# Performance work log

Measured on AMD Instinct MI355X. Metric: run time of the kernel, lower is better.

The kernel has to match this reference:

```python
import jax, jax.numpy as jnp
import numpy as np

B, SE, T, S, D, V = 64, 128, 64, 1024, 1024, 32000


def setup_inputs() -> dict:
    key = jax.random.key(0)
    ks = jax.random.split(key, 24)
    w = lambda k, shp: jax.random.normal(k, shp, jnp.float32) * 0.02
    return {
        "encoder_yts": jax.random.normal(ks[0], (B, SE, S), jnp.float32),
        "encoder_h": jax.random.normal(ks[1], (B, S), jnp.float32),
        "tgt": jax.random.randint(ks[2], (B, T), 0, V),
        "emb": w(ks[3], (V, D)),
        "asi_w": w(ks[4], (S, S)), "asi_b": jnp.zeros((S,), jnp.float32),
        "ayi_w": w(ks[5], (S, S)), "ayi_b": jnp.zeros((S,), jnp.float32),
        "aw_w": w(ks[6], (S, 1)), "aw_b": jnp.zeros((1,), jnp.float32),
        "wf_w": w(ks[7], (S, S)), "wf_b": jnp.zeros((S,), jnp.float32),
        "uf_w": w(ks[8], (D, S)), "uf_b": jnp.zeros((S,), jnp.float32),
        "wi_w": w(ks[9], (S, S)), "wi_b": jnp.zeros((S,), jnp.float32),
        "ui_w": w(ks[10], (D, S)), "ui_b": jnp.zeros((S,), jnp.float32),
        "wo_w": w(ks[11], (S, S)), "wo_b": jnp.zeros((S,), jnp.float32),
        "uo_w": w(ks[12], (D, S)), "uo_b": jnp.zeros((S,), jnp.float32),
        "wc_w": w(ks[13], (S, S)), "wc_b": jnp.zeros((S,), jnp.float32),
        "uc_w": w(ks[14], (D, S)), "uc_b": jnp.zeros((S,), jnp.float32),
        "xh_w": w(ks[15], (S, D)), "xh_b": jnp.zeros((D,), jnp.float32),
        "cls_w": w(ks[16], (D, V)), "cls_b": jnp.zeros((V,), jnp.float32),
    }


def reference(encoder_yts, encoder_h, tgt, emb,
              asi_w, asi_b, ayi_w, ayi_b, aw_w, aw_b,
              wf_w, wf_b, uf_w, uf_b, wi_w, wi_b, ui_w, ui_b,
              wo_w, wo_b, uo_w, uo_b, wc_w, wc_b, uc_w, uc_b,
              xh_w, xh_b, cls_w, cls_b):
    # Teacher-forced decode: xt at step i is the embedding of tgt[:, i].
    # Precompute attention key projection of encoder outputs: [B, SE, S]
    yts_proj = encoder_yts @ ayi_w + ayi_b
    xs = jnp.transpose(emb[tgt], (1, 0, 2))  # [T, B, D]

    def step(st, xt):
        # Additive attention (no tanh, matches source): e_ij = w^T(W si + U y)
        q = st @ asi_w + asi_b                       # [B, S]
        e = ((q[:, None, :] + yts_proj) @ aw_w)[..., 0] + aw_b[0]  # [B, SE]
        attn = jax.nn.softmax(e, axis=-1)            # [B, SE]
        ctx = jnp.einsum('be,bed->bd', attn, encoder_yts)  # [B, S] cell input
        # LSTM cell: note ct_1 is the fresh attention context each step
        ft = jax.nn.sigmoid(st @ wf_w + wf_b + xt @ uf_w + uf_b)
        it = jax.nn.sigmoid(st @ wi_w + wi_b + xt @ ui_w + ui_b)
        ot = jax.nn.sigmoid(st @ wo_w + wo_b + xt @ uo_w + uo_b)
        cbar = jnp.tanh(st @ wc_w + wc_b + xt @ uc_w + uc_b)
        ct = ft * ctx + it * cbar
        ht = ot * jnp.tanh(ct)                       # [B, S] -> next st
        logits = (ht @ xh_w + xh_b) @ cls_w + cls_b  # [B, V]
        pt = jax.nn.softmax(logits, axis=-1)
        return ht, (pt, attn)

    _, (pts, attns) = jax.lax.scan(step, encoder_h, xs)
    # [T,B,V] -> [B,T,V]; [T,B,SE] -> [B,T,SE]
    return jnp.transpose(pts, (1, 0, 2)), jnp.transpose(attns, (1, 0, 2))
```

## Files before the change

### kernel.cpp

```cpp
#include <hip/hip_runtime.h>
#include <cstdint>
#include <cstddef>

#define B_  64
#define SE_ 128
#define T_  64
#define S_  1024
#define D_  1024
#define V_  32000

typedef __attribute__((ext_vector_type(8))) short bhalf8;
typedef __attribute__((ext_vector_type(4))) float floatx4;

__device__ __forceinline__ float sigmoidf_(float x){ return 1.0f/(1.0f+__expf(-x)); }

__device__ __forceinline__ ushort f2bf(float f){
  uint32_t u = __float_as_uint(f);
  uint32_t r = (u + 0x7fffu + ((u >> 16) & 1u)) >> 16;
  return (ushort)r;
}
__device__ __forceinline__ float bf2f(ushort h){ return __uint_as_float(((uint32_t)h) << 16); }

__device__ __forceinline__ void glds16(const ushort* g, ushort* l){
  __builtin_amdgcn_global_load_lds((const __attribute__((address_space(1))) void*)g,
                                   (__attribute__((address_space(3))) void*)l, 16, 0, 0);
}

__device__ __forceinline__ float waveRedSum(float v){
  #pragma unroll
  for (int off = 32; off; off >>= 1) v += __shfl_down(v, off, 64);
  return v;
}


__global__ void k_attnvec(const float* __restrict__ ayi_w, const float* __restrict__ aw_w,
                          float* __restrict__ v){
  int wave = (blockIdx.x * blockDim.x + threadIdx.x) >> 6;
  int lane = threadIdx.x & 63;
  if (wave >= S_) return;
  const float* row = ayi_w + (size_t)wave * S_;
  float acc = 0.f;
  #pragma unroll 4
  for (int s = lane; s < S_; s += 64) acc += row[s] * aw_w[s];
  acc = waveRedSum(acc);
  if (lane == 0) v[wave] = acc;
}

__global__ void k_scores(const float* __restrict__ yts, const float* __restrict__ v,
                         float* __restrict__ scores){
  int wave = (blockIdx.x * blockDim.x + threadIdx.x) >> 6;
  int lane = threadIdx.x & 63;
  const float* row = yts + (size_t)wave * S_;
  float acc = 0.f;
  #pragma unroll 4
  for (int s = lane; s < S_; s += 64) acc += row[s] * v[s];
  acc = waveRedSum(acc);
  if (lane == 0) scores[wave] = acc;
}

__global__ void k_attn(const float* __restrict__ scores, float* __restrict__ attnw,
                       float* __restrict__ outAttn){
  int b = blockIdx.x;
  int e = threadIdx.x;
  __shared__ float sm[128];
  float x = scores[b*SE_ + e];
  sm[e] = x; __syncthreads();
  #pragma unroll
  for (int off = 64; off; off >>= 1){
    if (e < off) sm[e] = fmaxf(sm[e], sm[e+off]);
    __syncthreads();
  }
  float m = sm[0]; __syncthreads();
  float p = __expf(x - m);
  sm[e] = p; __syncthreads();
  #pragma unroll
  for (int off = 64; off; off >>= 1){
    if (e < off) sm[e] += sm[e+off];
    __syncthreads();
  }
  float a = p / sm[0];
  attnw[b*SE_ + e] = a;
  float* dst = outAttn + (size_t)b * T_ * SE_ + e;
  #pragma unroll 4
  for (int t = 0; t < T_; ++t) dst[t*SE_] = a;
}

__global__ void k_ctx(const float* __restrict__ yts, const float* __restrict__ attnw,
                      float* __restrict__ ctx){
  int idx = blockIdx.x * blockDim.x + threadIdx.x;
  int b = idx >> 10, s = idx & (S_-1);
  const float* base = yts + (size_t)b * SE_ * S_ + s;
  const float* a = attnw + b * SE_;
  float acc = 0.f;
  #pragma unroll 8
  for (int e = 0; e < SE_; ++e) acc += a[e] * base[(size_t)e * S_];
  ctx[idx] = acc;
}


__global__ void k_transcvt(const float* __restrict__ src, ushort* __restrict__ dst,
                           int K, int N){
  __shared__ float t[32][33];
  int n0 = blockIdx.x * 32, k0 = blockIdx.y * 32;
  for (int r = threadIdx.y; r < 32; r += 8)
    t[r][threadIdx.x] = src[(size_t)(k0 + r) * N + n0 + threadIdx.x];
  __syncthreads();
  for (int r = threadIdx.y; r < 32; r += 8)
    dst[(size_t)(n0 + r) * K + k0 + threadIdx.x] = f2bf(t[threadIdx.x][r]);
}

__global__ void k_cvt(const float* __restrict__ src, ushort* __restrict__ dst, int n4){
  int i = blockIdx.x * blockDim.x + threadIdx.x;
  if (i >= n4) return;
  float4 v = ((const float4*)src)[i];
  ushort4 o; o.x = f2bf(v.x); o.y = f2bf(v.y); o.z = f2bf(v.z); o.w = f2bf(v.w);
  ((ushort4*)dst)[i] = o;
}

__global__ void k_gathercvt(const float* __restrict__ emb, const int* __restrict__ tgt,
                            ushort* __restrict__ Xb){
  int r = blockIdx.x;
  int token = tgt[((r & 63) << 6) + (r >> 6)];
  const float4* src = (const float4*)(emb + (size_t)token * D_);
  ushort* dst = Xb + (size_t)r * D_;
  int i = threadIdx.x;
  float4 v = src[i];
  ushort4 o; o.x = f2bf(v.x); o.y = f2bf(v.y); o.z = f2bf(v.z); o.w = f2bf(v.w);
  ((ushort4*)dst)[i] = o;
}

__global__ void k_packbias(const float* __restrict__ wb0, const float* __restrict__ wb1,
                           const float* __restrict__ wb2, const float* __restrict__ wb3,
                           const float* __restrict__ ub0, const float* __restrict__ ub1,
                           const float* __restrict__ ub2, const float* __restrict__ ub3,
                           float* __restrict__ dst){
  int col = blockIdx.x * blockDim.x + threadIdx.x;
  int g = col >> 10, s = col & 1023;
  const float* wb = (g==0) ? wb0 : (g==1) ? wb1 : (g==2) ? wb2 : wb3;
  const float* ub = (g==0) ? ub0 : (g==1) ? ub1 : (g==2) ? ub2 : ub3;
  dst[col] = wb[s] + ub[s];
}

template<int OUT_MODE>
__global__ __launch_bounds__(256) void k_mfma_gemm(
    const ushort* __restrict__ A, const ushort* __restrict__ BT,
    const float* __restrict__ bias, void* __restrict__ C, int M, int N)
{
  __shared__ ushort As[128*32];
  __shared__ ushort Bs[128*32];
  const int tid = threadIdx.x;
  const int lane = tid & 63, w = tid >> 6;
  const int m0 = blockIdx.y * 128, n0 = blockIdx.x * 128;
  const int wr = (w >> 1) * 64, wc = (w & 1) * 64;

  const int cr = (lane >> 2);
  const int ck = (lane & 3) * 8;
  const ushort* gA0 = A  + (size_t)(m0 + (2*w)*16   + cr) * 1024 + ck;
  const ushort* gA1 = A  + (size_t)(m0 + (2*w+1)*16 + cr) * 1024 + ck;
  const ushort* gB0 = BT + (size_t)(n0 + (2*w)*16   + cr) * 1024 + ck;
  const ushort* gB1 = BT + (size_t)(n0 + (2*w+1)*16 + cr) * 1024 + ck;
  ushort* lA0 = As + (2*w)*512;   ushort* lA1 = As + (2*w+1)*512;
  ushort* lB0 = Bs + (2*w)*512;   ushort* lB1 = Bs + (2*w+1)*512;

  floatx4 acc[4][4] = {};

  for (int kt = 0; kt < 1024; kt += 32) {
    glds16(gA0 + kt, lA0); glds16(gA1 + kt, lA1);
    glds16(gB0 + kt, lB0); glds16(gB1 + kt, lB1);
    __syncthreads();
    bhalf8 a[4], b[4];
    #pragma unroll
    for (int f = 0; f < 4; ++f) {
      a[f] = *(const bhalf8*)&As[(wr + f*16 + (lane & 15)) * 32 + (lane >> 4) * 8];
      b[f] = *(const bhalf8*)&Bs[(wc + f*16 + (lane & 15)) * 32 + (lane >> 4) * 8];
    }
    #pragma unroll
    for (int i = 0; i < 4; ++i)
      #pragma unroll
      for (int j = 0; j < 4; ++j)
        acc[i][j] = __builtin_amdgcn_mfma_f32_16x16x32_bf16(a[i], b[j], acc[i][j], 0, 0, 0);
    __syncthreads();
  }

  const int crow = (lane >> 4) * 4, ccol = lane & 15;
  #pragma unroll
  for (int i = 0; i < 4; ++i) {
    #pragma unroll
    for (int j = 0; j < 4; ++j) {
      int row = m0 + wr + i*16 + crow;
      int col = n0 + wc + j*16 + ccol;
      float bv = bias ? bias[col] : 0.f;
      #pragma unroll
      for (int r = 0; r < 4; ++r) {
        float v = acc[i][j][r] + bv;
        if (OUT_MODE == 0) {
          ((float*)C)[(size_t)(row + r) * N + col] = v;
        } else if (OUT_MODE == 1) {
          int rr = row + r;
          ((float*)C)[(size_t)(((rr & 63) << 6) + (rr >> 6)) * N + col] = v;
        } else {
          ((ushort*)C)[(size_t)(row + r) * N + col] = f2bf(v);
        }
      }
    }
  }
}

__global__ __launch_bounds__(256) void k_step(
    const ushort* __restrict__ Hin,
    const ushort* __restrict__ WT,
    const ushort* __restrict__ preb,
    const float*  __restrict__ ctx,
    ushort* __restrict__ Hout)
{
  __shared__ ushort As[64*32];
  __shared__ ushort Bs[4][64*32];
  __shared__ float gbuf[4][64][66];
  const int tid = threadIdx.x, lane = tid & 63, w = tid >> 6;
  const int j = blockIdx.x;

  const int cr = (lane >> 2);
  const int ck = (lane & 3) * 8;
  const ushort* gA = Hin + (size_t)(w*16 + cr) * 1024 + ck;
  ushort* lA = As + w*512;
  const ushort* gB = WT + (size_t)(w*1024 + j*64 + cr) * 1024 + ck;
  ushort* lB = Bs[w];

  floatx4 acc[4][4] = {};

  for (int kt = 0; kt < 1024; kt += 32) {
    glds16(gA + kt, lA);
    #pragma unroll
    for (int c = 0; c < 4; ++c)
      glds16(gB + (size_t)(c*16)*1024 + kt, lB + c*512);
    __syncthreads();
    bhalf8 a[4], b[4];
    #pragma unroll
    for (int f = 0; f < 4; ++f) {
      a[f] = *(const bhalf8*)&As[(f*16 + (lane & 15)) * 32 + (lane >> 4) * 8];
      b[f] = *(const bhalf8*)&Bs[w][(f*16 + (lane & 15)) * 32 + (lane >> 4) * 8];
    }
    #pragma unroll
    for (int i = 0; i < 4; ++i)
      #pragma unroll
      for (int jj = 0; jj < 4; ++jj)
        acc[i][jj] = __builtin_amdgcn_mfma_f32_16x16x32_bf16(a[i], b[jj], acc[i][jj], 0, 0, 0);
    __syncthreads();
  }

  const int crow = (lane >> 4) * 4, ccol = lane & 15;
  #pragma unroll
  for (int i = 0; i < 4; ++i)
    #pragma unroll
    for (int jj = 0; jj < 4; ++jj)
      #pragma unroll
      for (int r = 0; r < 4; ++r)
        gbuf[w][i*16 + crow + r][jj*16 + ccol] = acc[i][jj][r];
  __syncthreads();

  for (int idx = tid; idx < 4096; idx += 256) {
    int b = idx >> 6, sp = idx & 63;
    int s = j*64 + sp;
    float fp = gbuf[0][b][sp] + bf2f(preb[b*4096 + s]);
    float ip = gbuf[1][b][sp] + bf2f(preb[b*4096 + 1024 + s]);
    float op = gbuf[2][b][sp] + bf2f(preb[b*4096 + 2048 + s]);
    float cp = gbuf[3][b][sp] + bf2f(preb[b*4096 + 3072 + s]);
    float ft = sigmoidf_(fp), it = sigmoidf_(ip), ot = sigmoidf_(op);
    float cb = tanhf(cp);
    float ct = ft * ctx[b*1024 + s] + it * cb;
    Hout[(size_t)b*1024 + s] = f2bf(ot * tanhf(ct));
  }
}

__global__ __launch_bounds__(256) void k_softmaxV(float* __restrict__ out){
  int row = blockIdx.x;
  float4* p = (float4*)(out + (size_t)row * V_);
  int tid = threadIdx.x;
  float m = -1e30f, ssum = 0.f;
  for (int i = tid; i < 8000; i += 256) {
    float4 v = p[i];
    float m4 = fmaxf(fmaxf(v.x, v.y), fmaxf(v.z, v.w));
    float mn = fmaxf(m, m4);
    ssum = ssum * __expf(m - mn)
         + __expf(v.x - mn) + __expf(v.y - mn) + __expf(v.z - mn) + __expf(v.w - mn);
    m = mn;
  }
  __shared__ float ms[256], ss[256];
  ms[tid] = m; ss[tid] = ssum; __syncthreads();
  #pragma unroll
  for (int off = 128; off; off >>= 1) {
    if (tid < off) {
      float m2 = fmaxf(ms[tid], ms[tid+off]);
      ss[tid] = ss[tid]*__expf(ms[tid]-m2) + ss[tid+off]*__expf(ms[tid+off]-m2);
      ms[tid] = m2;
    }
    __syncthreads();
  }
  float M = ms[0];
  float inv = 1.0f / ss[0];
  for (int i = tid; i < 8000; i += 256) {
    float4 v = p[i];
    v.x = __expf(v.x - M) * inv; v.y = __expf(v.y - M) * inv;
    v.z = __expf(v.z - M) * inv; v.w = __expf(v.w - M) * inv;
    p[i] = v;
  }
}


extern "C" void kernel_launch(void* const* d_in, const int* in_sizes, int n_in,
                              void* d_out, int out_size, void* d_ws, size_t ws_size,
                              hipStream_t stream){
  const float* yts   = (const float*)d_in[0];
  const float* enc_h = (const float*)d_in[1];
  const int*   tgt   = (const int*)d_in[2];
  const float* emb   = (const float*)d_in[3];
  const float* ayi_w = (const float*)d_in[6];
  const float* aw_w  = (const float*)d_in[8];
  const float* wf_w = (const float*)d_in[10]; const float* wf_b = (const float*)d_in[11];
  const float* uf_w = (const float*)d_in[12]; const float* uf_b = (const float*)d_in[13];
  const float* wi_w = (const float*)d_in[14]; const float* wi_b = (const float*)d_in[15];
  const float* ui_w = (const float*)d_in[16]; const float* ui_b = (const float*)d_in[17];
  const float* wo_w = (const float*)d_in[18]; const float* wo_b = (const float*)d_in[19];
  const float* uo_w = (const float*)d_in[20]; const float* uo_b = (const float*)d_in[21];
  const float* wc_w = (const float*)d_in[22]; const float* wc_b = (const float*)d_in[23];
  const float* uc_w = (const float*)d_in[24]; const float* uc_b = (const float*)d_in[25];
  const float* xh_w = (const float*)d_in[26]; const float* xh_b = (const float*)d_in[27];
  const float* cls_w= (const float*)d_in[28]; const float* cls_b= (const float*)d_in[29];

  float* out = (float*)d_out;
  float* outAttn = out + (size_t)B_ * T_ * V_;

  char* wsb = (char*)d_ws;
  size_t off = 0;
  auto alloc = [&](size_t bytes)->char*{
    char* p = wsb + off; off += (bytes + 255) & ~(size_t)255; return p;
  };
  ushort* clsT  = (ushort*)alloc((size_t)V_ * 1024 * 2);
  ushort* xhT   = (ushort*)alloc((size_t)1024 * 1024 * 2);
  ushort* WcatT = (ushort*)alloc((size_t)4096 * 1024 * 2);
  ushort* UcatT = (ushort*)alloc((size_t)4096 * 1024 * 2);
  float*  biasU = (float*)alloc(4096 * 4);
  float*  vvec  = (float*)alloc(S_ * 4);
  float*  scores= (float*)alloc(B_ * SE_ * 4);
  float*  attnw = (float*)alloc(B_ * SE_ * 4);
  float*  ctx   = (float*)alloc(B_ * S_ * 4);
  ushort* Xb    = (ushort*)alloc((size_t)4096 * 1024 * 2);
  ushort* preb  = (ushort*)alloc((size_t)4096 * 4096 * 2);
  ushort* Hst   = (ushort*)alloc((size_t)65 * 64 * 1024 * 2);
  if (off > ws_size) return;
  ushort* Zb = Xb;

  dim3 tb(32, 8);
  k_transcvt<<<dim3(V_/32, 32), tb, 0, stream>>>(cls_w, clsT, 1024, V_);
  k_transcvt<<<dim3(32, 32), tb, 0, stream>>>(xh_w, xhT, 1024, 1024);
  k_transcvt<<<dim3(32, 32), tb, 0, stream>>>(wf_w, WcatT + 0u*1048576u, 1024, 1024);
  k_transcvt<<<dim3(32, 32), tb, 0, stream>>>(wi_w, WcatT + 1u*1048576u, 1024, 1024);
  k_transcvt<<<dim3(32, 32), tb, 0, stream>>>(wo_w, WcatT + 2u*1048576u, 1024, 1024);
  k_transcvt<<<dim3(32, 32), tb, 0, stream>>>(wc_w, WcatT + 3u*1048576u, 1024, 1024);
  k_transcvt<<<dim3(32, 32), tb, 0, stream>>>(uf_w, UcatT + 0u*1048576u, 1024, 1024);
  k_transcvt<<<dim3(32, 32), tb, 0, stream>>>(ui_w, UcatT + 1u*1048576u, 1024, 1024);
  k_transcvt<<<dim3(32, 32), tb, 0, stream>>>(uo_w, UcatT + 2u*1048576u, 1024, 1024);
  k_transcvt<<<dim3(32, 32), tb, 0, stream>>>(uc_w, UcatT + 3u*1048576u, 1024, 1024);
  k_packbias<<<16, 256, 0, stream>>>(wf_b, wi_b, wo_b, wc_b, uf_b, ui_b, uo_b, uc_b, biasU);
  k_cvt<<<64, 256, 0, stream>>>(enc_h, Hst, 16384);
  k_gathercvt<<<4096, 256, 0, stream>>>(emb, tgt, Xb);

  k_attnvec<<<256, 256, 0, stream>>>(ayi_w, aw_w, vvec);
  k_scores<<<2048, 256, 0, stream>>>(yts, vvec, scores);
  k_attn<<<64, 128, 0, stream>>>(scores, attnw, outAttn);
  k_ctx<<<256, 256, 0, stream>>>(yts, attnw, ctx);

  k_mfma_gemm<2><<<dim3(32, 32), 256, 0, stream>>>(Xb, UcatT, biasU, preb, 4096, 4096);

  for (int t = 0; t < T_; ++t) {
    k_step<<<16, 256, 0, stream>>>(Hst + (size_t)t * 65536, WcatT,
                                   preb + (size_t)t * 262144, ctx,
                                   Hst + (size_t)(t+1) * 65536);
  }

  k_mfma_gemm<2><<<dim3(8, 32), 256, 0, stream>>>(Hst + 65536, xhT, xh_b, Zb, 4096, 1024);
  k_mfma_gemm<1><<<dim3(V_/128, 32), 256, 0, stream>>>(Zb, clsT, cls_b, out, 4096, V_);
  k_softmaxV<<<4096, 256, 0, stream>>>(out);
}
```

Measured before the change: 2.997 ms.

## Fuse recurrence into persistent cooperative kernel, swizzle GEMM blocks, cache softmax rows

The 64 per-step launches, each with 16 blocks, become one persistent cooperative kernel of 128 blocks. Each block keeps its 32 weight columns resident in swizzled LDS, splits K across waves, reduces the partial sums through LDS, and uses grid.sync between timesteps. This removes launch overhead, stops re-streaming the 8MB recurrent weight every step, and spreads the recurrence over more CUs, at the cost of a grid-wide barrier per step and reading H directly from global memory. The GEMM also gets a block-index remapping meant to improve cache locality, and the vocab softmax caches each row in 128KB of LDS so it does not re-read it from global memory.

```diff
diff --git a/kernel.cpp b/kernel.cpp
--- a/kernel.cpp
+++ b/kernel.cpp
@@ -1,4 +1,5 @@
 #include <hip/hip_runtime.h>
+#include <hip/hip_cooperative_groups.h>
 #include <cstdint>
 #include <cstddef>
 
@@ -150,7 +151,12 @@
   __shared__ ushort Bs[128*32];
   const int tid = threadIdx.x;
   const int lane = tid & 63, w = tid >> 6;
-  const int m0 = blockIdx.y * 128, n0 = blockIdx.x * 128;
+  const int nwg = gridDim.x * gridDim.y;
+  const int L = blockIdx.y * gridDim.x + blockIdx.x;
+  const int logical = (L & 7) * (nwg >> 3) + (L >> 3);
+  const int by = logical / gridDim.x;
+  const int bx = logical - by * gridDim.x;
+  const int m0 = by * 128, n0 = bx * 128;
   const int wr = (w >> 1) * 64, wc = (w & 1) * 64;
 
   const int cr = (lane >> 2);
@@ -206,79 +212,101 @@
   }
 }
 
-__global__ __launch_bounds__(256) void k_step(
-    const ushort* __restrict__ Hin,
-    const ushort* __restrict__ WT,
-    const ushort* __restrict__ preb,
-    const float*  __restrict__ ctx,
-    ushort* __restrict__ Hout)
+__global__ __launch_bounds__(512) void k_recur(
+    const ushort* __restrict__ WT, const ushort* __restrict__ preb,
+    const float* __restrict__ ctx, ushort* __restrict__ Hst)
 {
-  __shared__ ushort As[64*32];
-  __shared__ ushort Bs[4][64*32];
-  __shared__ float gbuf[4][64][66];
-  const int tid = threadIdx.x, lane = tid & 63, w = tid >> 6;
-  const int j = blockIdx.x;
-
-  const int cr = (lane >> 2);
-  const int ck = (lane & 3) * 8;
-  const ushort* gA = Hin + (size_t)(w*16 + cr) * 1024 + ck;
-  ushort* lA = As + w*512;
-  const ushort* gB = WT + (size_t)(w*1024 + j*64 + cr) * 1024 + ck;
-  ushort* lB = Bs[w];
-
-  floatx4 acc[4][4] = {};
-
-  for (int kt = 0; kt < 1024; kt += 32) {
-    glds16(gA + kt, lA);
-    #pragma unroll
-    for (int c = 0; c < 4; ++c)
-      glds16(gB + (size_t)(c*16)*1024 + kt, lB + c*512);
-    __syncthreads();
-    bhalf8 a[4], b[4];
-    #pragma unroll
-    for (int f = 0; f < 4; ++f) {
-      a[f] = *(const bhalf8*)&As[(f*16 + (lane & 15)) * 32 + (lane >> 4) * 8];
-      b[f] = *(const bhalf8*)&Bs[w][(f*16 + (lane & 15)) * 32 + (lane >> 4) * 8];
-    }
+  extern __shared__ char smem[];
+  float* gbuf = (float*)(smem + 65536);
+  const int tid  = threadIdx.x;
+  const int lane = tid & 63;
+  const int w    = tid >> 6;
+  const int kq   = w >> 1;
+  const int nh   = w & 1;
+  const int j    = blockIdx.x;
+
+  for (int it = tid; it < 4096; it += 512) {
+    int c = it >> 7, chunk = it & 127;
+    int g = c >> 3, sp = c & 7;
+    const uint4 v = *(const uint4*)(WT + (((size_t)(g*1024 + j*8 + sp)) << 10) + chunk*8);
+    *(uint4*)(smem + c*2048 + ((chunk*16) ^ ((c & 7) << 4))) = v;
+  }
+
+  const int cb  = tid >> 3, csp = tid & 7;
+  const float ctxv = ctx[(cb << 10) + j*8 + csp];
+
+  const int arow = lane & 15;
+  const int kof  = (lane >> 4) << 3;
+  const int bc   = (nh << 4) + (lane & 15);
+  const int bswz = (bc & 7) << 4;
+
+  cooperative_groups::grid_group grid = cooperative_groups::this_grid();
+  __syncthreads();
+
+  for (int t = 0; t < 64; ++t) {
+    const ushort* Hp = Hst + ((size_t)t << 16);
+    const ushort* prow = preb + (((size_t)(t*64 + cb)) << 12) + j*8 + csp;
+    ushort pg0 = prow[0], pg1 = prow[1024], pg2 = prow[2048], pg3 = prow[3072];
+
+    const ushort* Ab = Hp + kq*256 + kof;
+    floatx4 acc[4] = {};
+    bhalf8 af[2][4];
     #pragma unroll
     for (int i = 0; i < 4; ++i)
+      af[0][i] = *(const bhalf8*)(Ab + ((size_t)(i*16 + arow) << 10));
+    #pragma unroll
+    for (int i = 0; i < 4; ++i)
+      af[1][i] = *(const bhalf8*)(Ab + ((size_t)(i*16 + arow) << 10) + 32);
+    #pragma unroll
+    for (int ks = 0; ks < 8; ++ks) {
+      int k2 = (kq*256 + ks*32 + kof) * 2;
+      bhalf8 bf = *(const bhalf8*)(smem + bc*2048 + (k2 ^ bswz));
       #pragma unroll
-      for (int jj = 0; jj < 4; ++jj)
-        acc[i][jj] = __builtin_amdgcn_mfma_f32_16x16x32_bf16(a[i], b[jj], acc[i][jj], 0, 0, 0);
-    __syncthreads();
-  }
-
-  const int crow = (lane >> 4) * 4, ccol = lane & 15;
-  #pragma unroll
-  for (int i = 0; i < 4; ++i)
-    #pragma unroll
-    for (int jj = 0; jj < 4; ++jj)
+      for (int i = 0; i < 4; ++i)
+        acc[i] = __builtin_amdgcn_mfma_f32_16x16x32_bf16(af[ks & 1][i], bf, acc[i], 0, 0, 0);
+      if (ks < 6) {
+        #pragma unroll
+        for (int i = 0; i < 4; ++i)
+          af[ks & 1][i] = *(const bhalf8*)(Ab + ((size_t)(i*16 + arow) << 10) + (ks + 2)*32);
+      }
+    }
+    __syncthreads();
+    #pragma unroll
+    for (int i = 0; i < 4; ++i) {
+      int row = i*16 + ((lane >> 4) << 2);
       #pragma unroll
       for (int r = 0; r < 4; ++r)
-        gbuf[w][i*16 + crow + r][jj*16 + ccol] = acc[i][jj][r];
-  __syncthreads();
-
-  for (int idx = tid; idx < 4096; idx += 256) {
-    int b = idx >> 6, sp = idx & 63;
-    int s = j*64 + sp;
-    float fp = gbuf[0][b][sp] + bf2f(preb[b*4096 + s]);
-    float ip = gbuf[1][b][sp] + bf2f(preb[b*4096 + 1024 + s]);
-    float op = gbuf[2][b][sp] + bf2f(preb[b*4096 + 2048 + s]);
-    float cp = gbuf[3][b][sp] + bf2f(preb[b*4096 + 3072 + s]);
-    float ft = sigmoidf_(fp), it = sigmoidf_(ip), ot = sigmoidf_(op);
-    float cb = tanhf(cp);
-    float ct = ft * ctx[b*1024 + s] + it * cb;
-    Hout[(size_t)b*1024 + s] = f2bf(ot * tanhf(ct));
+        gbuf[kq*2112 + (row + r)*33 + bc] = acc[i][r];
+    }
+    __syncthreads();
+    {
+      float g0 = 0.f, g1 = 0.f, g2 = 0.f, g3 = 0.f;
+      #pragma unroll
+      for (int q = 0; q < 4; ++q) {
+        const float* gb = gbuf + q*2112 + cb*33;
+        g0 += gb[csp]; g1 += gb[8 + csp]; g2 += gb[16 + csp]; g3 += gb[24 + csp];
+      }
+      g0 += bf2f(pg0); g1 += bf2f(pg1); g2 += bf2f(pg2); g3 += bf2f(pg3);
+      float ft = sigmoidf_(g0), it_ = sigmoidf_(g1), ot = sigmoidf_(g2);
+      float cbar = tanhf(g3);
+      float ct = ft * ctxv + it_ * cbar;
+      Hst[((size_t)(t + 1) << 16) + (cb << 10) + j*8 + csp] = f2bf(ot * tanhf(ct));
+    }
+    __threadfence();
+    grid.sync();
   }
 }
 
 __global__ __launch_bounds__(256) void k_softmaxV(float* __restrict__ out){
-  int row = blockIdx.x;
-  float4* p = (float4*)(out + (size_t)row * V_);
+  extern __shared__ float rowbuf[];
+  int r = blockIdx.x;
+  float4* p = (float4*)(out + (size_t)r * V_);
+  float4* rb = (float4*)rowbuf;
   int tid = threadIdx.x;
   float m = -1e30f, ssum = 0.f;
   for (int i = tid; i < 8000; i += 256) {
     float4 v = p[i];
+    rb[i] = v;
     float m4 = fmaxf(fmaxf(v.x, v.y), fmaxf(v.z, v.w));
     float mn = fmaxf(m, m4);
     ssum = ssum * __expf(m - mn)
@@ -299,7 +327,7 @@
   float M = ms[0];
   float inv = 1.0f / ss[0];
   for (int i = tid; i < 8000; i += 256) {
-    float4 v = p[i];
+    float4 v = rb[i];
     v.x = __expf(v.x - M) * inv; v.y = __expf(v.y - M) * inv;
     v.z = __expf(v.z - M) * inv; v.w = __expf(v.w - M) * inv;
     p[i] = v;
@@ -372,13 +400,12 @@
 
   k_mfma_gemm<2><<<dim3(32, 32), 256, 0, stream>>>(Xb, UcatT, biasU, preb, 4096, 4096);
 
-  for (int t = 0; t < T_; ++t) {
-    k_step<<<16, 256, 0, stream>>>(Hst + (size_t)t * 65536, WcatT,
-                                   preb + (size_t)t * 262144, ctx,
-                                   Hst + (size_t)(t+1) * 65536);
+  {
+    void* args[] = { (void*)&WcatT, (void*)&preb, (void*)&ctx, (void*)&Hst };
+    hipLaunchCooperativeKernel((void*)k_recur, dim3(128), dim3(512), args, 99328, stream);
   }
 
   k_mfma_gemm<2><<<dim3(8, 32), 256, 0, stream>>>(Hst + 65536, xhT, xh_b, Zb, 4096, 1024);
   k_mfma_gemm<1><<<dim3(V_/128, 32), 256, 0, stream>>>(Zb, clsT, cls_b, out, 4096, V_);
-  k_softmaxV<<<4096, 256, 0, stream>>>(out);
-}
+  k_softmaxV<<<4096, 256, 128000, stream>>>(out);
+}
```

Result: slower. 4.121 ms (+37.5%).
